# Performance work log

Measured on AMD Instinct MI355X. Metric: run time of the kernel, lower is better.

Reference implementation:

```python
import jax, jax.numpy as jnp
import numpy as np

N, C, D_EMB = 4096, 8192, 512
SCALE = 3.0
KL_WEIGHT = 0.2


def _l2norm(x):
    # matches torch F.normalize(p=2, dim=-1) with eps clamp
    return x / jnp.maximum(jnp.linalg.norm(x, axis=-1, keepdims=True), 1e-12)


def setup_inputs() -> dict:
    key = jax.random.key(0)
    k1, k2, k3, k4 = jax.random.split(key, 4)
    X = jax.random.normal(k1, (N, D_EMB), dtype=jnp.float32)
    indices = jax.random.randint(k2, (N,), 0, N)
    T = jax.random.randint(k3, (N,), 0, C)
    proxies = jax.random.normal(k4, (C, D_EMB), dtype=jnp.float32) / 8.0
    sigmas_inv = jnp.full((C, D_EMB), np.log(np.e - 1.0), dtype=jnp.float32)
    return {"X": X, "indices": indices, "T": T, "proxies": proxies, "sigmas_inv": sigmas_inv}


def reference(X, indices, T, proxies, sigmas_inv):
    # per-class diagonal inverse-covariance weights s[c, d] = softplus(sigmas_inv)^2
    s = jax.nn.softplus(sigmas_inv) ** 2                        # (C, D)
    P = SCALE * _l2norm(proxies)                                # (C, D)
    Xn = SCALE * _l2norm(X)                                     # (N, D)
    # Mahalanobis-style distance D[n,c] = sum_d (x_nd - p_cd)^2 * s_cd
    Dmat = (Xn * Xn) @ s.T - 2.0 * (Xn @ (P * s).T) + jnp.sum(P * P * s, axis=-1)[None, :]  # (N, C)
    # log(softmax(-D)) == log_softmax(-D); one-hot targets (smoothing_const=0)
    logp = jax.nn.log_softmax(-Dmat, axis=-1)                   # (N, C)
    ce = -jnp.mean(logp[jnp.arange(Dmat.shape[0]), T])
    # KL regularizer: Sigma = 1/s, mu = normalized proxies
    Sig = 1.0 / s
    mus2 = _l2norm(proxies) ** 2
    kl = jnp.mean(jnp.sum(0.5 * (Sig + mus2 - 1.0 - jnp.log(Sig)), axis=-1))
    return ce + KL_WEIGHT * kl
```

## Files before the change

### kernel.cpp

```cpp
#include <hip/hip_runtime.h>
#include <hip/hip_bf16.h>
#include <cstdint>

#define N_ROWS 4096
#define N_CLS  8192
#define D_EMB  512
#define K_DIM  1024

using f32x4 = __attribute__((ext_vector_type(4))) float;

__device__ __forceinline__ float softplus_f(float v) {
  return (v > 20.f) ? v : log1pf(expf(v));
}

__device__ __forceinline__ unsigned short pack2_e4m3(float a, float b) {
  return (unsigned short)(__builtin_amdgcn_cvt_pk_fp8_f32(a, b, 0, false) & 0xffff);
}

__device__ __forceinline__ float block_sum256(float v) {
  __shared__ float red[4];
  #pragma unroll
  for (int o = 32; o; o >>= 1) v += __shfl_xor(v, o);
  __syncthreads();
  if ((threadIdx.x & 63) == 0) red[threadIdx.x >> 6] = v;
  __syncthreads();
  return red[0] + red[1] + red[2] + red[3];
}

__device__ __forceinline__ void global_to_lds16(const void* g, void* l) {
  const __attribute__((address_space(1))) unsigned int* gp =
      reinterpret_cast<const __attribute__((address_space(1))) unsigned int*>(
          reinterpret_cast<uintptr_t>(g));
  __attribute__((address_space(3))) unsigned int* lp =
      reinterpret_cast<__attribute__((address_space(3))) unsigned int*>(
          reinterpret_cast<uintptr_t>(l));
  __builtin_amdgcn_global_load_lds(gp, lp, 16, 0, 0);
}

__global__ __launch_bounds__(256) void k_prep(const float* __restrict__ proxies,
                                              const float* __restrict__ sigmas_inv,
                                              const float* __restrict__ X,
                                              unsigned char* __restrict__ Bmat,
                                              unsigned char* __restrict__ Amat,
                                              float* __restrict__ tvec,
                                              float* __restrict__ klc) {
  const int bid = blockIdx.x;
  const int tid = threadIdx.x;
  if (bid < N_CLS) {
    const int c = bid;
    const float* p  = proxies    + (size_t)c * D_EMB;
    const float* si = sigmas_inv + (size_t)c * D_EMB;
    float2 p2 = ((const float2*)p)[tid];
    float ss = block_sum256(p2.x * p2.x + p2.y * p2.y);
    float invn = 1.0f / fmaxf(sqrtf(ss), 1e-12f);
    float2 s2 = ((const float2*)si)[tid];
    float sp0 = softplus_f(s2.x), sp1 = softplus_f(s2.y);
    float s0 = sp0 * sp0, s1 = sp1 * sp1;
    float pn0 = p2.x * invn, pn1 = p2.y * invn;
    float P0 = 3.0f * pn0, P1 = 3.0f * pn1;
    unsigned short* brow = (unsigned short*)(Bmat + (size_t)c * K_DIM);
    brow[tid]       = pack2_e4m3(s0, s1);
    brow[256 + tid] = pack2_e4m3(P0 * s0, P1 * s1);
    float tc = P0 * P0 * s0 + P1 * P1 * s1;
    float kl = 0.5f * (1.0f / s0 + pn0 * pn0 - 1.0f + 2.0f * logf(sp0))
             + 0.5f * (1.0f / s1 + pn1 * pn1 - 1.0f + 2.0f * logf(sp1));
    tc = block_sum256(tc);
    kl = block_sum256(kl);
    if (tid == 0) { tvec[c] = tc; klc[c] = kl; }
  } else {
    const int n = bid - N_CLS;
    const float* x = X + (size_t)n * D_EMB;
    float2 x2 = ((const float2*)x)[tid];
    float ss = block_sum256(x2.x * x2.x + x2.y * x2.y);
    float invn = 3.0f / fmaxf(sqrtf(ss), 1e-12f);
    float v0 = x2.x * invn, v1 = x2.y * invn;
    unsigned short* arow = (unsigned short*)(Amat + (size_t)n * K_DIM);
    arow[tid]       = pack2_e4m3(-v0 * v0, -v1 * v1);
    arow[256 + tid] = pack2_e4m3(2.0f * v0, 2.0f * v1);
  }
}

__global__ __launch_bounds__(512, 4) void k_gemm_lse(const unsigned char* __restrict__ Amat,
                                                     const unsigned char* __restrict__ Bmat,
                                                     const float* __restrict__ tvec,
                                                     const int* __restrict__ T,
                                                     float* __restrict__ Pm,
                                                     float* __restrict__ Psum,
                                                     float* __restrict__ tgt) {
  union SMem {
    struct { unsigned char As[2][16384]; unsigned char Bs[2][8192]; } st;
    float ms[256][2][2];
  };
  __shared__ SMem sm;
  const int tid  = threadIdx.x;
  const int lane = tid & 63;
  const int wave = tid >> 6;
  const int wr = wave >> 1, wc = wave & 1;
  const int swz  = ((int)blockIdx.x & 7) * 128 + ((int)blockIdx.x >> 3);
  const int rt   = swz & 15;
  const int ct   = swz >> 4;
  const int row0 = rt * 256;
  const int col0 = ct * 128;

  f32x4 acc[4][4];
  #pragma unroll
  for (int i = 0; i < 4; ++i)
    #pragma unroll
    for (int j = 0; j < 4; ++j) acc[i][j] = (f32x4){0.f, 0.f, 0.f, 0.f};

  const int arow = wr * 64 + (lane & 15);
  const int bcol = wc * 64 + (lane & 15);
  const int kb8  = (lane >> 4) * 8;

  auto stage = [&](int buf, int ko) {
    #pragma unroll
    for (int rep = 0; rep < 2; ++rep) {
      int f  = rep * 8192 + tid * 16;
      int sf = f ^ (((f >> 7) & 7) << 4);
      global_to_lds16(Amat + (size_t)(row0 + (sf >> 6)) * K_DIM + ko + (sf & 63),
                      &sm.st.As[buf][f]);
    }
    {
      int f  = tid * 16;
      int sf = f ^ (((f >> 7) & 7) << 4);
      global_to_lds16(Bmat + (size_t)(col0 + (sf >> 6)) * K_DIM + ko + (sf & 63),
                      &sm.st.Bs[buf][f]);
    }
  };
  auto ld64 = [&](const unsigned char* base, int row, int kb) -> long {
    int f = row * 64 + kb;
    return *(const long*)(base + (f ^ (((f >> 7) & 7) << 4)));
  };

  stage(0, 0);
  __syncthreads();
  for (int t = 0; t < 16; ++t) {
    if (t < 15) stage((t + 1) & 1, (t + 1) * 64);
    const unsigned char* Ab = sm.st.As[t & 1];
    const unsigned char* Bb = sm.st.Bs[t & 1];
    __builtin_amdgcn_s_setprio(1);
    #pragma unroll
    for (int ks = 0; ks < 64; ks += 32) {
      long a[4], b[4];
      #pragma unroll
      for (int mi = 0; mi < 4; ++mi) a[mi] = ld64(Ab, arow + mi * 16, ks + kb8);
      #pragma unroll
      for (int ni = 0; ni < 4; ++ni) b[ni] = ld64(Bb, bcol + ni * 16, ks + kb8);
      #pragma unroll
      for (int mi = 0; mi < 4; ++mi)
        #pragma unroll
        for (int ni = 0; ni < 4; ++ni)
          acc[mi][ni] = __builtin_amdgcn_mfma_f32_16x16x32_fp8_fp8(a[mi], b[ni], acc[mi][ni], 0, 0, 0);
    }
    __builtin_amdgcn_s_setprio(0);
    __syncthreads();
  }

  const int l15 = lane & 15;
  float tc[4];
  #pragma unroll
  for (int ni = 0; ni < 4; ++ni)
    tc[ni] = tvec[col0 + wc * 64 + ni * 16 + l15];
  const int cbase = col0 + wc * 64 + l15;

  #pragma unroll
  for (int mi = 0; mi < 4; ++mi) {
    #pragma unroll
    for (int j = 0; j < 4; ++j) {
      const int grow = row0 + wr * 64 + mi * 16 + ((lane >> 4) << 2) + j;
      const int d = T[grow] - cbase;
      float z0 = acc[mi][0][j] - tc[0];
      float z1 = acc[mi][1][j] - tc[1];
      float z2 = acc[mi][2][j] - tc[2];
      float z3 = acc[mi][3][j] - tc[3];
      if (d == 0)  tgt[grow] = z0;
      if (d == 16) tgt[grow] = z1;
      if (d == 32) tgt[grow] = z2;
      if (d == 48) tgt[grow] = z3;
      float m = fmaxf(fmaxf(z0, z1), fmaxf(z2, z3));
      #pragma unroll
      for (int o = 1; o < 16; o <<= 1) m = fmaxf(m, __shfl_xor(m, o));
      float s = __expf(z0 - m) + __expf(z1 - m) + __expf(z2 - m) + __expf(z3 - m);
      #pragma unroll
      for (int o = 1; o < 16; o <<= 1) s += __shfl_xor(s, o);
      if (l15 == 0) {
        int rloc = wr * 64 + mi * 16 + ((lane >> 4) << 2) + j;
        sm.ms[rloc][wc][0] = m;
        sm.ms[rloc][wc][1] = s;
      }
    }
  }
  __syncthreads();
  if (tid < 256) {
    float m0 = sm.ms[tid][0][0], s0 = sm.ms[tid][0][1];
    float m1 = sm.ms[tid][1][0], s1 = sm.ms[tid][1][1];
    float M = fmaxf(m0, m1);
    float S = s0 * __expf(m0 - M) + s1 * __expf(m1 - M);
    Pm  [(size_t)(row0 + tid) * 64 + ct] = M;
    Psum[(size_t)(row0 + tid) * 64 + ct] = S;
  }
}

__global__ __launch_bounds__(256) void k_red(const float* __restrict__ Pm,
                                             const float* __restrict__ Psum,
                                             const float* __restrict__ tgt,
                                             const float* __restrict__ klc,
                                             float* __restrict__ cep,
                                             float* __restrict__ klp) {
  const int b = blockIdx.x;
  const int tid = threadIdx.x;
  const int n = b * 16 + (tid >> 4);
  const int l4 = tid & 15;
  float4 pm = *(const float4*)(Pm   + (size_t)n * 64 + l4 * 4);
  float4 ps = *(const float4*)(Psum + (size_t)n * 64 + l4 * 4);
  float m = fmaxf(fmaxf(pm.x, pm.y), fmaxf(pm.z, pm.w));
  #pragma unroll
  for (int o = 1; o < 16; o <<= 1) m = fmaxf(m, __shfl_xor(m, o));
  float S = ps.x * __expf(pm.x - m) + ps.y * __expf(pm.y - m)
          + ps.z * __expf(pm.z - m) + ps.w * __expf(pm.w - m);
  #pragma unroll
  for (int o = 1; o < 16; o <<= 1) S += __shfl_xor(S, o);
  float ce = (l4 == 0) ? (m + logf(S) - tgt[n]) : 0.f;
  float kl = (tid < 32) ? klc[b * 32 + tid] : 0.f;
  ce = block_sum256(ce);
  kl = block_sum256(kl);
  if (tid == 0) { cep[b] = ce; klp[b] = kl; }
}

__global__ __launch_bounds__(256) void k_fin2(const float* __restrict__ cep,
                                              const float* __restrict__ klp,
                                              float* __restrict__ out) {
  const int tid = threadIdx.x;
  float ce = block_sum256(cep[tid]);
  float kl = block_sum256(klp[tid]);
  if (tid == 0) out[0] = ce / (float)N_ROWS + 0.2f * (kl / (float)N_CLS);
}

extern "C" void kernel_launch(void* const* d_in, const int* in_sizes, int n_in,
                              void* d_out, int out_size, void* d_ws, size_t ws_size,
                              hipStream_t stream) {
  const float* X          = (const float*)d_in[0];
  const int*   T          = (const int*)d_in[2];
  const float* proxies    = (const float*)d_in[3];
  const float* sigmas_inv = (const float*)d_in[4];

  char* ws = (char*)d_ws;
  unsigned char* Amat = (unsigned char*)ws;
  unsigned char* Bmat = (unsigned char*)(ws + (4u << 20));
  float* tvec = (float*)(ws + (12u << 20));
  float* klc  = (float*)(ws + (12u << 20) + (32u << 10));
  float* Pm   = (float*)(ws + (12u << 20) + (64u << 10));
  float* Psum = (float*)(ws + (13u << 20) + (64u << 10));
  float* tgt  = (float*)(ws + (14u << 20) + (64u << 10));
  float* cep  = (float*)(ws + (14u << 20) + (80u << 10));
  float* klp  = (float*)(ws + (14u << 20) + (84u << 10));
  float* out  = (float*)d_out;

  hipLaunchKernelGGL(k_prep,     dim3(N_CLS + N_ROWS), dim3(256), 0, stream,
                     proxies, sigmas_inv, X, Bmat, Amat, tvec, klc);
  hipLaunchKernelGGL(k_gemm_lse, dim3(1024),           dim3(512), 0, stream,
                     Amat, Bmat, tvec, T, Pm, Psum, tgt);
  hipLaunchKernelGGL(k_red,      dim3(256),            dim3(256), 0, stream,
                     Pm, Psum, tgt, klc, cep, klp);
  hipLaunchKernelGGL(k_fin2,     dim3(1),              dim3(256), 0, stream,
                     cep, klp, out);
}
```

Before: 88.90 us.

## Triple-buffer GEMM LDS staging with interleaved quadrant MFMA schedule

Replaces the double-buffered K loop with a triple-buffered, fully unrolled schedule. The next-next tile's A and B loads are issued in the middle of each iteration, and the 4x4 MFMA block is split into four 2x2 quadrants with LDS reads and s_barriers in between, so global loads, LDS reads and MFMAs overlap. Target labels are also read once per row group as an int4 in the epilogue. LDS use grows to 72KB, which may lower occupancy below the declared 4 blocks per CU, and the many barriers add synchronisation overhead.

```diff
diff --git a/kernel.cpp b/kernel.cpp
--- a/kernel.cpp
+++ b/kernel.cpp
@@ -36,6 +36,9 @@
           reinterpret_cast<uintptr_t>(l));
   __builtin_amdgcn_global_load_lds(gp, lp, 16, 0, 0);
 }
+
+#define LGKM0() do { asm volatile("s_waitcnt lgkmcnt(0)" ::: "memory"); \
+                     __builtin_amdgcn_sched_barrier(0); } while (0)
 
 __global__ __launch_bounds__(256) void k_prep(const float* __restrict__ proxies,
                                               const float* __restrict__ sigmas_inv,
@@ -87,11 +90,7 @@
                                                      float* __restrict__ Pm,
                                                      float* __restrict__ Psum,
                                                      float* __restrict__ tgt) {
-  union SMem {
-    struct { unsigned char As[2][16384]; unsigned char Bs[2][8192]; } st;
-    float ms[256][2][2];
-  };
-  __shared__ SMem sm;
+  __shared__ __align__(16) unsigned char lds[73728];
   const int tid  = threadIdx.x;
   const int lane = tid & 63;
   const int wave = tid >> 6;
@@ -112,50 +111,94 @@
   const int bcol = wc * 64 + (lane & 15);
   const int kb8  = (lane >> 4) * 8;
 
-  auto stage = [&](int buf, int ko) {
-    #pragma unroll
-    for (int rep = 0; rep < 2; ++rep) {
-      int f  = rep * 8192 + tid * 16;
-      int sf = f ^ (((f >> 7) & 7) << 4);
-      global_to_lds16(Amat + (size_t)(row0 + (sf >> 6)) * K_DIM + ko + (sf & 63),
-                      &sm.st.As[buf][f]);
-    }
-    {
-      int f  = tid * 16;
-      int sf = f ^ (((f >> 7) & 7) << 4);
-      global_to_lds16(Bmat + (size_t)(col0 + (sf >> 6)) * K_DIM + ko + (sf & 63),
-                      &sm.st.Bs[buf][f]);
-    }
+  const int f0  = tid * 16;
+  const int sf0 = f0 ^ (((f0 >> 7) & 7) << 4);
+  const unsigned char* gA0 = Amat + (size_t)(row0 + (sf0 >> 6)) * K_DIM + (sf0 & 63);
+  const unsigned char* gB0 = Bmat + (size_t)(col0 + (sf0 >> 6)) * K_DIM + (sf0 & 63);
+
+  auto stageA = [&](int slot, int ko) {
+    unsigned char* base = lds + slot * 24576;
+    global_to_lds16(gA0 + ko,          base + f0);
+    global_to_lds16(gA0 + 131072 + ko, base + 8192 + f0);
+  };
+  auto stageB = [&](int slot, int ko) {
+    global_to_lds16(gB0 + ko, lds + slot * 24576 + 16384 + f0);
   };
   auto ld64 = [&](const unsigned char* base, int row, int kb) -> long {
     int f = row * 64 + kb;
     return *(const long*)(base + (f ^ (((f >> 7) & 7) << 4)));
   };
 
-  stage(0, 0);
-  __syncthreads();
-  for (int t = 0; t < 16; ++t) {
-    if (t < 15) stage((t + 1) & 1, (t + 1) * 64);
-    const unsigned char* Ab = sm.st.As[t & 1];
-    const unsigned char* Bb = sm.st.Bs[t & 1];
-    __builtin_amdgcn_s_setprio(1);
-    #pragma unroll
-    for (int ks = 0; ks < 64; ks += 32) {
-      long a[4], b[4];
-      #pragma unroll
-      for (int mi = 0; mi < 4; ++mi) a[mi] = ld64(Ab, arow + mi * 16, ks + kb8);
-      #pragma unroll
-      for (int ni = 0; ni < 4; ++ni) b[ni] = ld64(Bb, bcol + ni * 16, ks + kb8);
-      #pragma unroll
-      for (int mi = 0; mi < 4; ++mi)
-        #pragma unroll
-        for (int ni = 0; ni < 4; ++ni)
-          acc[mi][ni] = __builtin_amdgcn_mfma_f32_16x16x32_fp8_fp8(a[mi], b[ni], acc[mi][ni], 0, 0, 0);
-    }
-    __builtin_amdgcn_s_setprio(0);
-    __syncthreads();
+  stageA(0, 0);  stageB(0, 0);
+  stageA(1, 64); stageB(1, 64);
+  asm volatile("s_waitcnt vmcnt(3)" ::: "memory");
+  __builtin_amdgcn_sched_barrier(0);
+  __builtin_amdgcn_s_barrier();
+
+  long a01[4], a23[4], b01[4], b23[4];
+
+#define GITER(T_, NW) { \
+    const unsigned char* S  = lds + ((T_) % 3) * 24576; \
+    const unsigned char* Sb = S + 16384; \
+     \
+    a01[0] = ld64(S,  arow,      kb8); a01[1] = ld64(S,  arow,      32 + kb8); \
+    a01[2] = ld64(S,  arow + 16, kb8); a01[3] = ld64(S,  arow + 16, 32 + kb8); \
+    b01[0] = ld64(Sb, bcol,      kb8); b01[1] = ld64(Sb, bcol,      32 + kb8); \
+    b01[2] = ld64(Sb, bcol + 16, kb8); b01[3] = ld64(Sb, bcol + 16, 32 + kb8); \
+    if ((T_) + 2 < 16) stageA(((T_) + 2) % 3, ((T_) + 2) * 64); \
+    __builtin_amdgcn_s_barrier(); \
+    LGKM0(); \
+    __builtin_amdgcn_s_setprio(1); \
+    _Pragma("unroll") for (int mi = 0; mi < 2; ++mi) \
+      _Pragma("unroll") for (int ni = 0; ni < 2; ++ni) \
+        _Pragma("unroll") for (int ks = 0; ks < 2; ++ks) \
+          acc[mi][ni] = __builtin_amdgcn_mfma_f32_16x16x32_fp8_fp8(a01[mi*2+ks], b01[ni*2+ks], acc[mi][ni], 0, 0, 0); \
+    __builtin_amdgcn_s_setprio(0); \
+    __builtin_amdgcn_s_barrier(); \
+     \
+    b23[0] = ld64(Sb, bcol + 32, kb8); b23[1] = ld64(Sb, bcol + 32, 32 + kb8); \
+    b23[2] = ld64(Sb, bcol + 48, kb8); b23[3] = ld64(Sb, bcol + 48, 32 + kb8); \
+    if ((T_) + 2 < 16) stageB(((T_) + 2) % 3, ((T_) + 2) * 64); \
+    __builtin_amdgcn_s_barrier(); \
+    LGKM0(); \
+    __builtin_amdgcn_s_setprio(1); \
+    _Pragma("unroll") for (int mi = 0; mi < 2; ++mi) \
+      _Pragma("unroll") for (int ni = 0; ni < 2; ++ni) \
+        _Pragma("unroll") for (int ks = 0; ks < 2; ++ks) \
+          acc[mi][2+ni] = __builtin_amdgcn_mfma_f32_16x16x32_fp8_fp8(a01[mi*2+ks], b23[ni*2+ks], acc[mi][2+ni], 0, 0, 0); \
+    __builtin_amdgcn_s_setprio(0); \
+    __builtin_amdgcn_s_barrier(); \
+     \
+    a23[0] = ld64(S, arow + 32, kb8); a23[1] = ld64(S, arow + 32, 32 + kb8); \
+    a23[2] = ld64(S, arow + 48, kb8); a23[3] = ld64(S, arow + 48, 32 + kb8); \
+    __builtin_amdgcn_s_barrier(); \
+    LGKM0(); \
+    __builtin_amdgcn_s_setprio(1); \
+    _Pragma("unroll") for (int mi = 0; mi < 2; ++mi) \
+      _Pragma("unroll") for (int ni = 0; ni < 2; ++ni) \
+        _Pragma("unroll") for (int ks = 0; ks < 2; ++ks) \
+          acc[2+mi][2+ni] = __builtin_amdgcn_mfma_f32_16x16x32_fp8_fp8(a23[mi*2+ks], b23[ni*2+ks], acc[2+mi][2+ni], 0, 0, 0); \
+    __builtin_amdgcn_s_setprio(0); \
+    __builtin_amdgcn_s_barrier(); \
+     \
+    __builtin_amdgcn_s_setprio(1); \
+    _Pragma("unroll") for (int mi = 0; mi < 2; ++mi) \
+      _Pragma("unroll") for (int ni = 0; ni < 2; ++ni) \
+        _Pragma("unroll") for (int ks = 0; ks < 2; ++ks) \
+          acc[2+mi][ni] = __builtin_amdgcn_mfma_f32_16x16x32_fp8_fp8(a23[mi*2+ks], b01[ni*2+ks], acc[2+mi][ni], 0, 0, 0); \
+    __builtin_amdgcn_s_setprio(0); \
+    asm volatile("s_waitcnt vmcnt(" #NW ")" ::: "memory"); \
+    __builtin_amdgcn_sched_barrier(0); \
+    __builtin_amdgcn_s_barrier(); \
   }
 
+  GITER(0, 3)  GITER(1, 3)  GITER(2, 3)  GITER(3, 3)
+  GITER(4, 3)  GITER(5, 3)  GITER(6, 3)  GITER(7, 3)
+  GITER(8, 3)  GITER(9, 3)  GITER(10, 3) GITER(11, 3)
+  GITER(12, 3) GITER(13, 3) GITER(14, 0) GITER(15, 0)
+#undef GITER
+
+  float (*ms)[2][2] = (float (*)[2][2])lds;
   const int l15 = lane & 15;
   float tc[4];
   #pragma unroll
@@ -165,18 +208,20 @@
 
   #pragma unroll
   for (int mi = 0; mi < 4; ++mi) {
+    const int rowb = row0 + wr * 64 + mi * 16 + ((lane >> 4) << 2);
+    int4 tv4 = *(const int4*)(T + rowb);
+    int tvj[4] = {tv4.x, tv4.y, tv4.z, tv4.w};
     #pragma unroll
     for (int j = 0; j < 4; ++j) {
-      const int grow = row0 + wr * 64 + mi * 16 + ((lane >> 4) << 2) + j;
-      const int d = T[grow] - cbase;
+      const int d = tvj[j] - cbase;
       float z0 = acc[mi][0][j] - tc[0];
       float z1 = acc[mi][1][j] - tc[1];
       float z2 = acc[mi][2][j] - tc[2];
       float z3 = acc[mi][3][j] - tc[3];
-      if (d == 0)  tgt[grow] = z0;
-      if (d == 16) tgt[grow] = z1;
-      if (d == 32) tgt[grow] = z2;
-      if (d == 48) tgt[grow] = z3;
+      if (d == 0)  tgt[rowb + j] = z0;
+      if (d == 16) tgt[rowb + j] = z1;
+      if (d == 32) tgt[rowb + j] = z2;
+      if (d == 48) tgt[rowb + j] = z3;
       float m = fmaxf(fmaxf(z0, z1), fmaxf(z2, z3));
       #pragma unroll
       for (int o = 1; o < 16; o <<= 1) m = fmaxf(m, __shfl_xor(m, o));
@@ -185,15 +230,15 @@
       for (int o = 1; o < 16; o <<= 1) s += __shfl_xor(s, o);
       if (l15 == 0) {
         int rloc = wr * 64 + mi * 16 + ((lane >> 4) << 2) + j;
-        sm.ms[rloc][wc][0] = m;
-        sm.ms[rloc][wc][1] = s;
+        ms[rloc][wc][0] = m;
+        ms[rloc][wc][1] = s;
       }
     }
   }
   __syncthreads();
   if (tid < 256) {
-    float m0 = sm.ms[tid][0][0], s0 = sm.ms[tid][0][1];
-    float m1 = sm.ms[tid][1][0], s1 = sm.ms[tid][1][1];
+    float m0 = ms[tid][0][0], s0 = ms[tid][0][1];
+    float m1 = ms[tid][1][0], s1 = ms[tid][1][1];
     float M = fmaxf(m0, m1);
     float S = s0 * __expf(m0 - M) + s1 * __expf(m1 - M);
     Pm  [(size_t)(row0 + tid) * 64 + ct] = M;
```

Result: slower. 93.36 us (+5.0%).
